# Kernel tuning notes

Measured on AMD Instinct MI355X. Metric: run time of the kernel, lower is better.

## Reference

```python
import jax, jax.numpy as jnp
import numpy as np

B, I, L, D, E, H, HR, A = 4096, 512, 128, 512, 8, 512, 256, 32


def setup_inputs() -> dict:
    key = jax.random.key(0)
    ks = jax.random.split(key, 12)
    s = 0.05
    n = lambda k, shape: (jax.random.normal(k, shape, jnp.float32) * s)
    return {
        "x": jax.random.normal(ks[0], (B, I), jnp.float32),
        "lang_embs": jax.random.normal(ks[1], (B, L), jnp.float32),
        "h_router": jnp.zeros((B, HR), jnp.float32),
        "h_experts": jnp.zeros((E, B, H), jnp.float32),
        # input projection Linear(I+L -> D)
        "W_in": n(ks[2], (D, I + L)), "b_in": jnp.zeros((D,), jnp.float32),
        # router GRU cell (PyTorch layout: rows ordered [r, z, n])
        "Wih_r": n(ks[3], (3 * HR, D)), "Whh_r": n(ks[4], (3 * HR, HR)),
        "bih_r": jnp.zeros((3 * HR,), jnp.float32), "bhh_r": jnp.zeros((3 * HR,), jnp.float32),
        # router fc Linear(HR -> E)
        "W_fc": n(ks[5], (E, HR)), "b_fc": jnp.zeros((E,), jnp.float32),
        # stacked expert GRU cells
        "Wih_e": n(ks[6], (E, 3 * H, D)), "Whh_e": n(ks[7], (E, 3 * H, H)),
        "bih_e": jnp.zeros((E, 3 * H), jnp.float32), "bhh_e": jnp.zeros((E, 3 * H), jnp.float32),
        # stacked expert projections Linear(H -> D)
        "W_proj": n(ks[8], (E, D, H)), "b_proj": jnp.zeros((E, D), jnp.float32),
        # head Linear(D -> A)
        "W_head": n(ks[9], (A, D)), "b_head": jnp.zeros((A,), jnp.float32),
    }


def _gru_cell(gx, gh, h):
    """Single GRU step given precomputed input/hidden gate pre-activations.
    gx, gh: (..., 3H) ordered [r, z, n]; h: (..., H)."""
    Hh = h.shape[-1]
    r = jax.nn.sigmoid(gx[..., :Hh] + gh[..., :Hh])
    z = jax.nn.sigmoid(gx[..., Hh:2 * Hh] + gh[..., Hh:2 * Hh])
    nct = jnp.tanh(gx[..., 2 * Hh:] + r * gh[..., 2 * Hh:])
    return (1.0 - z) * nct + z * h


def reference(x, lang_embs, h_router, h_experts,
              W_in, b_in, Wih_r, Whh_r, bih_r, bhh_r, W_fc, b_fc,
              Wih_e, Whh_e, bih_e, bhh_e, W_proj, b_proj, W_head, b_head):
    # input projection: (B, I+L) -> (B, D)
    xp = jnp.concatenate([x, lang_embs], axis=1) @ W_in.T + b_in

    # router GRU step + softmax weights
    gx_r = xp @ Wih_r.T + bih_r                      # (B, 3HR)
    gh_r = h_router @ Whh_r.T + bhh_r                # (B, 3HR)
    h_router_new = _gru_cell(gx_r, gh_r, h_router)   # (B, HR)
    weights = jax.nn.softmax(h_router_new @ W_fc.T + b_fc, axis=-1)  # (B, E)

    # all expert GRU steps fused into batched einsums over the expert dim
    gx_e = jnp.einsum('bd,egd->ebg', xp, Wih_e) + bih_e[:, None, :]        # (E, B, 3H)
    gh_e = jnp.einsum('ebh,egh->ebg', h_experts, Whh_e) + bhh_e[:, None, :]
    h_experts_new = _gru_cell(gx_e, gh_e, h_experts)                        # (E, B, H)

    # per-expert projection back to intermediate dim, then router-weighted sum
    expert_out = jnp.einsum('ebh,edh->ebd', h_experts_new, W_proj) + b_proj[:, None, :]
    combined = jnp.einsum('ebd,be->bd', expert_out, weights)               # (B, D)

    logits = combined @ W_head.T + b_head                                  # (B, A)
    return (logits, h_router_new, h_experts_new)
```

## Files before the change

### kernel.cpp

```cpp
#include <hip/hip_runtime.h>
#include <cstddef>
#include <cstdint>

#define B_  4096
#define I_  512
#define L_  128
#define D_  512
#define E_  8
#define H_  512
#define HR_ 256
#define A_  32

typedef __attribute__((ext_vector_type(8))) __bf16 bf16x8;
typedef __attribute__((ext_vector_type(4))) __bf16 bf16x4;
typedef __attribute__((ext_vector_type(4))) float floatx4;

__device__ __forceinline__ float sigmoidf_(float x) { return 1.0f / (1.0f + __expf(-x)); }

__device__ __forceinline__ void load_lds16(const void* g, void* l) {
    __builtin_amdgcn_global_load_lds((__attribute__((address_space(1))) void*)g,
                                     (__attribute__((address_space(3))) void*)l, 16, 0, 0);
}

struct HiLo { __bf16 h, l; };
__device__ __forceinline__ HiLo hi_lo(float v) {
    HiLo r;
    r.h = (__bf16)v;
    r.l = (__bf16)(v - (float)r.h);
    return r;
}
__device__ __forceinline__ void split4(float4 v, bf16x4& hi, bf16x4& lo) {
    HiLo a = hi_lo(v.x), b = hi_lo(v.y), c = hi_lo(v.z), d = hi_lo(v.w);
    hi = (bf16x4){a.h, b.h, c.h, d.h};
    lo = (bf16x4){a.l, b.l, c.l, d.l};
}

__global__ __launch_bounds__(256) void f2b_k(const float* __restrict__ src,
                                             __bf16* __restrict__ dst, int n4) {
    int i = blockIdx.x * 256 + threadIdx.x;
    if (i < n4) {
        float4 v = ((const float4*)src)[i];
        bf16x4 o = { (__bf16)v.x, (__bf16)v.y, (__bf16)v.z, (__bf16)v.w };
        *(bf16x4*)(dst + (size_t)i * 4) = o;
    }
}

__global__ __launch_bounds__(256) void wcat2_k(const float* __restrict__ W,
                                               __bf16* __restrict__ out,
                                               int K4, int n4tot) {
    int i4 = blockIdx.x * 256 + threadIdx.x;
    if (i4 >= n4tot) return;
    int row = i4 / K4;
    int c4  = i4 - row * K4;
    const int K = K4 * 4;
    float4 v = ((const float4*)W)[i4];
    bf16x4 hi, lo;
    split4(v, hi, lo);
    __bf16* dst = out + (size_t)row * 2 * K + c4 * 4;
    *(bf16x4*)(dst)     = hi;
    *(bf16x4*)(dst + K) = lo;
}

__global__ __launch_bounds__(256) void concat_cat_k(const float* __restrict__ x,
                                                    const float* __restrict__ lang,
                                                    __bf16* __restrict__ out) {
    int idx = blockIdx.x * 256 + threadIdx.x;
    int b = idx / 160;
    int c = idx - b * 160;
    float4 v;
    if (c < 128) v = ((const float4*)x)[(size_t)b * 128 + c];
    else         v = ((const float4*)lang)[(size_t)b * 32 + (c - 128)];
    bf16x4 hi, lo;
    split4(v, hi, lo);
    __bf16* dst = out + (size_t)b * 1920 + c * 4;
    *(bf16x4*)(dst)        = hi;
    *(bf16x4*)(dst + 640)  = hi;
    *(bf16x4*)(dst + 1280) = lo;
}

__global__ __launch_bounds__(256) void split2cat_k(const float* __restrict__ src,
                                                   __bf16* __restrict__ out) {
    int i4 = blockIdx.x * 256 + threadIdx.x;
    int b = i4 >> 7;
    int c4 = i4 & 127;
    float4 v = ((const float4*)src)[i4];
    bf16x4 hi, lo;
    split4(v, hi, lo);
    __bf16* dst = out + (size_t)b * 1536 + c4 * 4;
    *(bf16x4*)(dst)         = hi;
    *(bf16x4*)(dst + 512)   = hi;
    *(bf16x4*)(dst + 1024)  = lo;
}

__global__ __launch_bounds__(256) void f2bhe_k(const float* __restrict__ he,
                                               __bf16* __restrict__ dst, int r0) {
    int i4 = blockIdx.x * 256 + threadIdx.x;
    int e   = i4 >> 18;
    int rem = i4 & 262143;
    int row = rem >> 7;
    int c4  = rem & 127;
    float4 v = ((const float4*)he)[(size_t)e * (B_ * 128) + (size_t)(r0 + row) * 128 + c4];
    bf16x4 o = { (__bf16)v.x, (__bf16)v.y, (__bf16)v.z, (__bf16)v.w };
    *(bf16x4*)(dst + (size_t)i4 * 4) = o;
}

template<int MODE, bool XORD>
__global__ __launch_bounds__(256) void mgemm(
    const __bf16* __restrict__ A, long long aBatch,
    const __bf16* __restrict__ Bw, long long bBatch, int bRS, int kWrap,
    const float* __restrict__ bias, long long biasBatch,
    float* __restrict__ Cv, long long cBatch,
    int N, int K,
    const float* __restrict__ scale, int sstride, int szBatch)
{
    constexpr int ASZ = 128 * 32;
    __shared__ __align__(16) __bf16 As[2 * ASZ];
    __shared__ __align__(16) __bf16 Bs[2 * ASZ];

    const int tid  = threadIdx.x;
    const int w    = tid >> 6;
    const int lane = tid & 63;
    const int m0 = (XORD ? blockIdx.z : blockIdx.x) * 128;
    const int n0 = blockIdx.y * 128;
    const int z  = XORD ? blockIdx.x : blockIdx.z;

    const int lrow = lane >> 2;
    const int lseg = lane & 3;
    const __bf16* Ag0 = A + (size_t)z * aBatch + (size_t)(m0 + w * 32 + lrow) * K + lseg * 8;
    const __bf16* Ag1 = Ag0 + (size_t)16 * K;
    const __bf16* Bg0 = Bw + (size_t)z * bBatch + (size_t)(n0 + w * 32 + lrow) * bRS + lseg * 8;
    const __bf16* Bg1 = Bg0 + (size_t)16 * bRS;

    const int wm = w & 1, wn = w >> 1;
    const int lr16 = lane & 15;
    const int lq   = lane >> 4;

    floatx4 acc[4][4];
#pragma unroll
    for (int i = 0; i < 4; ++i)
#pragma unroll
        for (int j = 0; j < 4; ++j) acc[i][j] = (floatx4){0.f, 0.f, 0.f, 0.f};

    const int NSTEP = K >> 5;

    auto STAGE = [&](int s, int buf) {
        const int k0 = s << 5;
        const int kb = (k0 < kWrap) ? k0 : (k0 - kWrap);
        __bf16* al = As + buf * ASZ + (w * 32) * 32;
        __bf16* bl = Bs + buf * ASZ + (w * 32) * 32;
        load_lds16(Ag0 + k0, al);
        load_lds16(Ag1 + k0, al + 16 * 32);
        load_lds16(Bg0 + kb, bl);
        load_lds16(Bg1 + kb, bl + 16 * 32);
    };

    int cur = 0;
    STAGE(0, 0);
    __syncthreads();
    for (int s = 0; s < NSTEP; ++s) {
        if (s + 1 < NSTEP) STAGE(s + 1, cur ^ 1);

        const __bf16* Af = As + cur * ASZ + (wm * 64 + lr16) * 32 + lq * 8;
        const __bf16* Bf = Bs + cur * ASZ + (wn * 64 + lr16) * 32 + lq * 8;
        bf16x8 af[4], bfr[4];
#pragma unroll
        for (int t = 0; t < 4; ++t) {
            af[t]  = *(const bf16x8*)(Af + t * 16 * 32);
            bfr[t] = *(const bf16x8*)(Bf + t * 16 * 32);
        }
#pragma unroll
        for (int tm = 0; tm < 4; ++tm)
#pragma unroll
            for (int tn = 0; tn < 4; ++tn)
                acc[tm][tn] = __builtin_amdgcn_mfma_f32_16x16x32_bf16(af[tm], bfr[tn], acc[tm][tn], 0, 0, 0);

        __syncthreads();
        cur ^= 1;
    }

    const float* biasz = bias + (size_t)z * biasBatch;
    const int sz = z * szBatch;
#pragma unroll
    for (int tm = 0; tm < 4; ++tm) {
        const int mbase = m0 + wm * 64 + tm * 16 + lq * 4;
#pragma unroll
        for (int r = 0; r < 4; ++r) {
            const int m = mbase + r;
            float wsc = 0.f;
            if (MODE == 2) wsc = scale[(size_t)m * sstride + sz];
#pragma unroll
            for (int tn = 0; tn < 4; ++tn) {
                const int n = n0 + wn * 64 + tn * 16 + lr16;
                float v = acc[tm][tn][r] + biasz[n];
                const size_t ci = (size_t)z * cBatch + (size_t)m * N + n;
                if (MODE == 0) Cv[ci] = v;
                else           Cv[ci] = wsc * v;
            }
        }
    }
}

template<int HD, bool WRITE_HNEW, bool XORD>
__global__ __launch_bounds__(256) void fgru(
    const __bf16* __restrict__ Ab, long long aBatch,
    const __bf16* __restrict__ Whh, long long wBatch,
    const float* __restrict__ bhh, long long bhhBatch,
    const float* __restrict__ gx, long long gxBatch,
    const float* __restrict__ hprev, long long hBatch,
    float* __restrict__ hout, long long hoBatch,
    __bf16* __restrict__ hnew, long long hnBatch)
{
    __shared__ __align__(16) __bf16 As[128 * 32];
    __shared__ __align__(16) __bf16 Bs[192 * 32];

    const int tid  = threadIdx.x;
    const int w    = tid >> 6;
    const int lane = tid & 63;
    const int m0 = (XORD ? blockIdx.z : blockIdx.x) * 128;
    const int j0 = blockIdx.y * 64;
    const int z  = XORD ? blockIdx.x : blockIdx.z;

    const int lrow = lane >> 2;
    const int lseg = lane & 3;
    const __bf16* Ag0 = Ab + (size_t)z * aBatch + (size_t)(m0 + w * 32 + lrow) * HD + lseg * 8;
    const __bf16* Ag1 = Ag0 + (size_t)16 * HD;
    __bf16* Al0 = As + (w * 32) * 32;
    __bf16* Al1 = Al0 + 16 * 32;

    const __bf16* Wz = Whh + (size_t)z * wBatch;
    const __bf16* Bg[3];
    __bf16* Bl[3];
#pragma unroll
    for (int i = 0; i < 3; ++i) {
        const int r = (w * 3 + i) * 16 + lrow;
        const int gate = r >> 6;
        const int grow = gate * HD + j0 + (r & 63);
        Bg[i] = Wz + (size_t)grow * HD + lseg * 8;
        Bl[i] = Bs + ((w * 3 + i) * 16) * 32;
    }

    const int mh = w & 1, nh = w >> 1;
    const int lr16 = lane & 15;
    const int lq   = lane >> 4;
    const __bf16* Af = As + (mh * 64 + lr16) * 32 + lq * 8;
    const __bf16* Bf = Bs + (nh * 32 + lr16) * 32 + lq * 8;

    floatx4 acc[3][4][2];
#pragma unroll
    for (int g = 0; g < 3; ++g)
#pragma unroll
        for (int i = 0; i < 4; ++i)
#pragma unroll
            for (int j = 0; j < 2; ++j) acc[g][i][j] = (floatx4){0.f, 0.f, 0.f, 0.f};

    for (int k0 = 0; k0 < HD; k0 += 32) {
        __syncthreads();
        load_lds16(Ag0 + k0, Al0);
        load_lds16(Ag1 + k0, Al1);
#pragma unroll
        for (int i = 0; i < 3; ++i) load_lds16(Bg[i] + k0, Bl[i]);
        __syncthreads();

        bf16x8 af[4], bf[3][2];
#pragma unroll
        for (int t = 0; t < 4; ++t) af[t] = *(const bf16x8*)(Af + t * 16 * 32);
#pragma unroll
        for (int g = 0; g < 3; ++g)
#pragma unroll
            for (int tn = 0; tn < 2; ++tn)
                bf[g][tn] = *(const bf16x8*)(Bf + (g * 64 + tn * 16) * 32);
#pragma unroll
        for (int g = 0; g < 3; ++g)
#pragma unroll
            for (int tm = 0; tm < 4; ++tm)
#pragma unroll
                for (int tn = 0; tn < 2; ++tn)
                    acc[g][tm][tn] = __builtin_amdgcn_mfma_f32_16x16x32_bf16(af[tm], bf[g][tn], acc[g][tm][tn], 0, 0, 0);
    }

    const float* bhhz = bhh + (size_t)z * bhhBatch;
#pragma unroll
    for (int tm = 0; tm < 4; ++tm) {
#pragma unroll
        for (int rr = 0; rr < 4; ++rr) {
            const int row = m0 + mh * 64 + tm * 16 + lq * 4 + rr;
            const float* gxrow = gx + (size_t)z * gxBatch + (size_t)row * (3 * HD);
            const float* hrow  = hprev + (size_t)z * hBatch + (size_t)row * HD;
#pragma unroll
            for (int tn = 0; tn < 2; ++tn) {
                const int j = j0 + nh * 32 + tn * 16 + lr16;
                float ghr = acc[0][tm][tn][rr] + bhhz[j];
                float ghz = acc[1][tm][tn][rr] + bhhz[HD + j];
                float ghn = acc[2][tm][tn][rr] + bhhz[2 * HD + j];
                float r  = sigmoidf_(gxrow[j] + ghr);
                float zz = sigmoidf_(gxrow[HD + j] + ghz);
                float n  = tanhf(gxrow[2 * HD + j] + r * ghn);
                float hv = hrow[j];
                float o  = (1.f - zz) * n + zz * hv;
                hout[(size_t)z * hoBatch + (size_t)row * HD + j] = o;
                if (WRITE_HNEW)
                    hnew[(size_t)z * hnBatch + (size_t)row * HD + j] = (__bf16)o;
            }
        }
    }
}

template<int MROWS>
__global__ __launch_bounds__(256, 2) void fxgru_k(
    const __bf16* __restrict__ xpc,
    const __bf16* __restrict__ Wih,
    const float* __restrict__ bih,
    const __bf16* __restrict__ heb,
    const __bf16* __restrict__ Whh,
    const float* __restrict__ bhh,
    const float* __restrict__ hprev,
    long long hBatch,
    float* __restrict__ hout,
    long long hoBatch,
    __bf16* __restrict__ hnew)
{
    constexpr int ASZ = 128 * 32;
    constexpr int BSZ = 192 * 32;
    __shared__ __align__(16) __bf16 As[2 * ASZ];
    __shared__ __align__(16) __bf16 Bs[2 * BSZ];

    const int tid  = threadIdx.x;
    const int w    = tid >> 6;
    const int lane = tid & 63;
    const int z  = blockIdx.x;
    const int j0 = blockIdx.y * 64;
    const int m0 = blockIdx.z * 128;

    const int lrow = lane >> 2;
    const int lseg = lane & 3;
    const int aoff = (w * 32) * 32;
    int BlOff[3];
#pragma unroll
    for (int i = 0; i < 3; ++i) BlOff[i] = ((w * 3 + i) * 16) * 32;

    const int mh = w & 1, nh = w >> 1;
    const int lr16 = lane & 15;
    const int lq   = lane >> 4;

    floatx4 acc[3][4][2];
    floatx4 accn[4][2];
#pragma unroll
    for (int g = 0; g < 3; ++g)
#pragma unroll
        for (int i = 0; i < 4; ++i)
#pragma unroll
            for (int j = 0; j < 2; ++j) acc[g][i][j] = (floatx4){0.f, 0.f, 0.f, 0.f};
#pragma unroll
    for (int i = 0; i < 4; ++i)
#pragma unroll
        for (int j = 0; j < 2; ++j) accn[i][j] = (floatx4){0.f, 0.f, 0.f, 0.f};

    auto COMPA = [&](int buf) {
        const __bf16* Af = As + buf * ASZ + (mh * 64 + lr16) * 32 + lq * 8;
        const __bf16* Bf = Bs + buf * BSZ + (nh * 32 + lr16) * 32 + lq * 8;
        bf16x8 af[4], bf[3][2];
#pragma unroll
        for (int t = 0; t < 4; ++t) af[t] = *(const bf16x8*)(Af + t * 16 * 32);
#pragma unroll
        for (int g = 0; g < 3; ++g)
#pragma unroll
            for (int tn = 0; tn < 2; ++tn)
                bf[g][tn] = *(const bf16x8*)(Bf + (g * 64 + tn * 16) * 32);
#pragma unroll
        for (int g = 0; g < 3; ++g)
#pragma unroll
            for (int tm = 0; tm < 4; ++tm)
#pragma unroll
                for (int tn = 0; tn < 2; ++tn)
                    acc[g][tm][tn] = __builtin_amdgcn_mfma_f32_16x16x32_bf16(af[tm], bf[g][tn], acc[g][tm][tn], 0, 0, 0);
    };
    auto COMPB = [&](int buf) {
        const __bf16* Af = As + buf * ASZ + (mh * 64 + lr16) * 32 + lq * 8;
        const __bf16* Bf = Bs + buf * BSZ + (nh * 32 + lr16) * 32 + lq * 8;
        bf16x8 af[4], bf[3][2];
#pragma unroll
        for (int t = 0; t < 4; ++t) af[t] = *(const bf16x8*)(Af + t * 16 * 32);
#pragma unroll
        for (int g = 0; g < 3; ++g)
#pragma unroll
            for (int tn = 0; tn < 2; ++tn)
                bf[g][tn] = *(const bf16x8*)(Bf + (g * 64 + tn * 16) * 32);
#pragma unroll
        for (int tm = 0; tm < 4; ++tm)
#pragma unroll
            for (int tn = 0; tn < 2; ++tn) {
                acc[0][tm][tn] = __builtin_amdgcn_mfma_f32_16x16x32_bf16(af[tm], bf[0][tn], acc[0][tm][tn], 0, 0, 0);
                acc[1][tm][tn] = __builtin_amdgcn_mfma_f32_16x16x32_bf16(af[tm], bf[1][tn], acc[1][tm][tn], 0, 0, 0);
                accn[tm][tn]   = __builtin_amdgcn_mfma_f32_16x16x32_bf16(af[tm], bf[2][tn], accn[tm][tn], 0, 0, 0);
            }
    };

    int cur = 0;
    {
        const __bf16* AgA0 = xpc + (size_t)(m0 + w * 32 + lrow) * 1536 + lseg * 8;
        const __bf16* AgA1 = AgA0 + (size_t)16 * 1536;
        const __bf16* WihZ = Wih + (size_t)z * (1536 * 1024);
        const __bf16* BgA[3];
#pragma unroll
        for (int i = 0; i < 3; ++i) {
            const int r = (w * 3 + i) * 16 + lrow;
            const int grow = (r >> 6) * 512 + j0 + (r & 63);
            BgA[i] = WihZ + (size_t)grow * 1024 + lseg * 8;
        }
        auto STAGE_A = [&](int s, int buf) {
            const int k0 = s << 5;
            const int kb = (k0 < 1024) ? k0 : (k0 - 1024);
            __bf16* al = As + buf * ASZ + aoff;
            __bf16* bl = Bs + buf * BSZ;
            load_lds16(AgA0 + k0, al);
            load_lds16(AgA1 + k0, al + 16 * 32);
#pragma unroll
            for (int i = 0; i < 3; ++i) load_lds16(BgA[i] + kb, bl + BlOff[i]);
        };

        STAGE_A(0, 0);
        __syncthreads();
        for (int s = 0; s < 47; ++s) {
            STAGE_A(s + 1, cur ^ 1);
            COMPA(cur);
            __syncthreads();
            cur ^= 1;
        }
    }
    {
        const __bf16* AgB0 = heb + (size_t)z * (MROWS * 512)
                                 + (size_t)(m0 + w * 32 + lrow) * 512 + lseg * 8;
        const __bf16* AgB1 = AgB0 + (size_t)16 * 512;
        const __bf16* WhhZ = Whh + (size_t)z * (1536 * 512);
        const __bf16* BgB[3];
#pragma unroll
        for (int i = 0; i < 3; ++i) {
            const int r = (w * 3 + i) * 16 + lrow;
            const int grow = (r >> 6) * 512 + j0 + (r & 63);
            BgB[i] = WhhZ + (size_t)grow * 512 + lseg * 8;
        }
        auto STAGE_B = [&](int t, int buf) {
            const int k0 = t << 5;
            __bf16* al = As + buf * ASZ + aoff;
            __bf16* bl = Bs + buf * BSZ;
            load_lds16(AgB0 + k0, al);
            load_lds16(AgB1 + k0, al + 16 * 32);
#pragma unroll
            for (int i = 0; i < 3; ++i) load_lds16(BgB[i] + k0, bl + BlOff[i]);
        };

        STAGE_B(0, cur ^ 1);
        COMPA(cur);
        __syncthreads();
        cur ^= 1;
        for (int t = 0; t < 16; ++t) {
            if (t + 1 < 16) STAGE_B(t + 1, cur ^ 1);
            COMPB(cur);
            __syncthreads();
            cur ^= 1;
        }
    }

    const float* bihz = bih + (size_t)z * 1536;
    const float* bhhz = bhh + (size_t)z * 1536;
#pragma unroll
    for (int tm = 0; tm < 4; ++tm) {
#pragma unroll
        for (int rr = 0; rr < 4; ++rr) {
            const int row = m0 + mh * 64 + tm * 16 + lq * 4 + rr;
            const float* hrow = hprev + (size_t)z * hBatch + (size_t)row * 512;
#pragma unroll
            for (int tn = 0; tn < 2; ++tn) {
                const int j = j0 + nh * 32 + tn * 16 + lr16;
                float gr  = acc[0][tm][tn][rr] + bihz[j] + bhhz[j];
                float gz  = acc[1][tm][tn][rr] + bihz[512 + j] + bhhz[512 + j];
                float gxn = acc[2][tm][tn][rr] + bihz[1024 + j];
                float ghn = accn[tm][tn][rr] + bhhz[1024 + j];
                float r  = sigmoidf_(gr);
                float zz = sigmoidf_(gz);
                float n  = tanhf(gxn + r * ghn);
                float hv = hrow[j];
                float o  = (1.f - zz) * n + zz * hv;
                hout[(size_t)z * hoBatch + (size_t)row * 512 + j] = o;
                hnew[(size_t)z * (MROWS * 512) + (size_t)row * 512 + j] = (__bf16)o;
            }
        }
    }
}

__global__ __launch_bounds__(256) void fc_softmax_k(const float* __restrict__ hr,
                                                    const float* __restrict__ Wfc,
                                                    const float* __restrict__ bfc,
                                                    float* __restrict__ wts) {
    int lane = threadIdx.x & 63;
    int wave = threadIdx.x >> 6;
    int rg = lane >> 3;
    int e  = lane & 7;
    int b  = blockIdx.x * 32 + wave * 8 + rg;
    const float* h = hr + (size_t)b * HR_;
    const float* w = Wfc + (size_t)e * HR_;
    float acc = 0.0f;
#pragma unroll 4
    for (int k = 0; k < HR_; k += 4) {
        float4 hv = *(const float4*)(h + k);
        float4 wv = *(const float4*)(w + k);
        acc += hv.x * wv.x + hv.y * wv.y + hv.z * wv.z + hv.w * wv.w;
    }
    acc += bfc[e];
    float m = acc;
    for (int off = 4; off; off >>= 1) m = fmaxf(m, __shfl_xor(m, off, 8));
    float ex = __expf(acc - m);
    float s = ex;
    for (int off = 4; off; off >>= 1) s += __shfl_xor(s, off, 8);
    wts[(size_t)b * E_ + e] = ex / s;
}

__global__ __launch_bounds__(256) void reduce8_k(const float* __restrict__ P,
                                                 float* __restrict__ comb,
                                                 int n4, int ps4) {
    int i = blockIdx.x * 256 + threadIdx.x;
    if (i >= n4) return;
    float4 s = ((const float4*)P)[i];
#pragma unroll
    for (int e = 1; e < E_; ++e) {
        float4 v = ((const float4*)P)[i + (size_t)e * ps4];
        s.x += v.x; s.y += v.y; s.z += v.z; s.w += v.w;
    }
    ((float4*)comb)[i] = s;
}

__global__ __launch_bounds__(256) void head_k(const float* __restrict__ comb,
                                              const float* __restrict__ Wh,
                                              const float* __restrict__ bh,
                                              float* __restrict__ out) {
    __shared__ float hs[8][512];
    int b0 = blockIdx.x * 8;
    for (int i = threadIdx.x; i < 8 * 128; i += 256) {
        int rr = i >> 7, cc = i & 127;
        ((float4*)hs[rr])[cc] = ((const float4*)(comb + (size_t)(b0 + rr) * 512))[cc];
    }
    __syncthreads();
    int r = threadIdx.x >> 5, c = threadIdx.x & 31;
    const float* wrow = Wh + (size_t)c * 512;
    float acc = 0.f;
    for (int k = 0; k < 512; k += 4) {
        float4 wv = *(const float4*)(wrow + k);
        float4 hv = *(const float4*)(&hs[r][k]);
        acc += hv.x * wv.x + hv.y * wv.y + hv.z * wv.z + hv.w * wv.w;
    }
    out[(size_t)(b0 + r) * 32 + c] = acc + bh[c];
}

extern "C" void kernel_launch(void* const* d_in, const int* in_sizes, int n_in,
                              void* d_out, int out_size, void* d_ws, size_t ws_size,
                              hipStream_t stream)
{
    const float* x      = (const float*)d_in[0];
    const float* lang   = (const float*)d_in[1];
    const float* h_r    = (const float*)d_in[2];
    const float* h_e    = (const float*)d_in[3];
    const float* W_in   = (const float*)d_in[4];
    const float* b_in   = (const float*)d_in[5];
    const float* Wih_r  = (const float*)d_in[6];
    const float* Whh_r  = (const float*)d_in[7];
    const float* bih_r  = (const float*)d_in[8];
    const float* bhh_r  = (const float*)d_in[9];
    const float* W_fc   = (const float*)d_in[10];
    const float* b_fc   = (const float*)d_in[11];
    const float* Wih_e  = (const float*)d_in[12];
    const float* Whh_e  = (const float*)d_in[13];
    const float* bih_e  = (const float*)d_in[14];
    const float* bhh_e  = (const float*)d_in[15];
    const float* W_proj = (const float*)d_in[16];
    const float* b_proj = (const float*)d_in[17];
    const float* W_head = (const float*)d_in[18];
    const float* b_head = (const float*)d_in[19];

    float* out_logits = (float*)d_out;
    float* out_hr     = out_logits + (size_t)B_ * A_;
    float* out_he     = out_hr + (size_t)B_ * HR_;

    char* wsb = (char*)d_ws;
    size_t off = 0;
    auto alloc = [&](size_t bytes) -> char* {
        char* p = wsb + off;
        off = (off + bytes + 255) & ~(size_t)255;
        return p;
    };

    __bf16* Wih_e_hl = (__bf16*)alloc((size_t)12288 * 1024 * 2);
    __bf16* Whh_e_b  = (__bf16*)alloc((size_t)8 * 1536 * 512 * 2);
    __bf16* W_proj_b = (__bf16*)alloc((size_t)8 * 512 * 512 * 2);
    __bf16* xp_cat   = (__bf16*)alloc((size_t)B_ * 1536 * 2);
    float*  wts      = (float*)alloc((size_t)B_ * E_ * 4);
    float*  comb     = (float*)alloc((size_t)B_ * D_ * 4);

    char* R = wsb + off;
    __bf16* W_in_hl  = (__bf16*)(R);
    __bf16* Wih_r_hl = (__bf16*)(R + 1310720);
    __bf16* Whh_r_b  = (__bf16*)(R + 1310720 + 1572864);
    __bf16* hr_b     = (__bf16*)(R + 1310720 + 1572864 + 393216);
    char*   Rp       = R + 1310720 + 1572864 + 393216 + 2097152;
    __bf16* xcat_cat = (__bf16*)(Rp);
    float*  xp       = (float*)(Rp + 15728640);
    float*  gxr      = (float*)(Rp + 15728640 + 8388608);
    float*  Pch      = (float*)(R);
    __bf16* hebch    = (__bf16*)(R + 33554432);
    __bf16* henewch  = (__bf16*)(R + 33554432 + 16777216);

    wcat2_k<<<(512 * 160 + 255) / 256, 256, 0, stream>>>(W_in, W_in_hl, 160, 512 * 160);
    wcat2_k<<<(768 * 128 + 255) / 256, 256, 0, stream>>>(Wih_r, Wih_r_hl, 128, 768 * 128);
    wcat2_k<<<(12288 * 128 + 255) / 256, 256, 0, stream>>>(Wih_e, Wih_e_hl, 128, 12288 * 128);
    f2b_k<<<(49152 + 255) / 256, 256, 0, stream>>>(Whh_r, Whh_r_b, 49152);
    f2b_k<<<(1572864 + 255) / 256, 256, 0, stream>>>(Whh_e, Whh_e_b, 1572864);
    f2b_k<<<(524288 + 255) / 256, 256, 0, stream>>>(W_proj, W_proj_b, 524288);
    f2b_k<<<(262144 + 255) / 256, 256, 0, stream>>>(h_r, hr_b, 262144);

    concat_cat_k<<<(B_ * 160) / 256, 256, 0, stream>>>(x, lang, xcat_cat);
    mgemm<0, false><<<dim3(32, 4, 1), 256, 0, stream>>>(xcat_cat, 0, W_in_hl, 0, 1280, 1280,
                                                        b_in, 0, xp, 0, D_, 1920, nullptr, 0, 0);
    split2cat_k<<<(B_ * 128) / 256, 256, 0, stream>>>(xp, xp_cat);

    mgemm<0, false><<<dim3(32, 6, 1), 256, 0, stream>>>(xp_cat, 0, Wih_r_hl, 0, 1024, 1024,
                                                        bih_r, 0, gxr, 0, 3 * HR_, 1536, nullptr, 0, 0);
    fgru<HR_, false, false><<<dim3(32, 4, 1), 256, 0, stream>>>(
        hr_b, 0, Whh_r_b, 0, bhh_r, 0, gxr, 0, h_r, 0, out_hr, 0, nullptr, 0);
    fc_softmax_k<<<B_ / 32, 256, 0, stream>>>(out_hr, W_fc, b_fc, wts);

    for (int c = 0; c < 2; ++c) {
        const int r0 = c * 2048;
        f2bhe_k<<<(8 * 2048 * 128) / 256, 256, 0, stream>>>(h_e, hebch, r0);
        fxgru_k<2048><<<dim3(8, 8, 16), 256, 0, stream>>>(
            xp_cat + (size_t)r0 * 1536,
            Wih_e_hl, bih_e,
            hebch, Whh_e_b, bhh_e,
            h_e + (size_t)r0 * H_, (long long)B_ * H_,
            out_he + (size_t)r0 * H_, (long long)B_ * H_,
            henewch);
        mgemm<2, true><<<dim3(8, 4, 16), 256, 0, stream>>>(
            henewch, (long long)2048 * H_,
            W_proj_b, (long long)D_ * H_, 512, 512,
            b_proj, D_,
            Pch, (long long)2048 * D_, D_, H_,
            wts + (size_t)r0 * E_, E_, 1);
        reduce8_k<<<(2048 * 128 + 255) / 256, 256, 0, stream>>>(
            Pch, comb + (size_t)r0 * D_, 2048 * 128, 2048 * 128);
    }

    head_k<<<B_ / 8, 256, 0, stream>>>(comb, W_head, b_head, out_logits);
}
```

Baseline: 719.7 us.

## Triple-buffer LDS tiles in fused expert GRU GEMM with vmcnt-based waits

Expands the shared-memory A/B tile buffers from two to three stages and prefetches two tiles ahead. Full __syncthreads are replaced with explicit vmcnt waits plus raw barriers, so async global-to-LDS loads overlap longer with MFMA compute. The input-gate and hidden-gate phases are chained through the same ring buffer with an explicit drain at the end. This costs more LDS per block, which could limit occupancy, and relies on correct hand-counted vmcnt values.

Measured after the change: 675.8 us. 1.06x faster.

```diff
diff --git a/kernel.cpp b/kernel.cpp
--- a/kernel.cpp
+++ b/kernel.cpp
@@ -321,8 +321,8 @@
 {
     constexpr int ASZ = 128 * 32;
     constexpr int BSZ = 192 * 32;
-    __shared__ __align__(16) __bf16 As[2 * ASZ];
-    __shared__ __align__(16) __bf16 Bs[2 * BSZ];
+    __shared__ __align__(16) __bf16 As[3 * ASZ];
+    __shared__ __align__(16) __bf16 Bs[3 * BSZ];
 
     const int tid  = threadIdx.x;
     const int w    = tid >> 6;
@@ -395,6 +395,16 @@
             }
     };
 
+#define TILE_WAIT(N) do { \
+        asm volatile("s_waitcnt vmcnt(" #N ")" ::: "memory"); \
+        __builtin_amdgcn_s_barrier(); \
+        __builtin_amdgcn_sched_barrier(0); \
+    } while (0)
+#define READ_DONE() do { \
+        __builtin_amdgcn_sched_barrier(0); \
+        __builtin_amdgcn_s_barrier(); \
+    } while (0)
+
     int cur = 0;
     {
         const __bf16* AgA0 = xpc + (size_t)(m0 + w * 32 + lrow) * 1536 + lseg * 8;
@@ -419,12 +429,14 @@
         };
 
         STAGE_A(0, 0);
-        __syncthreads();
-        for (int s = 0; s < 47; ++s) {
-            STAGE_A(s + 1, cur ^ 1);
+        STAGE_A(1, 1);
+        STAGE_A(2, 2);
+        for (int s = 0; s < 45; ++s) {
+            TILE_WAIT(10);
             COMPA(cur);
-            __syncthreads();
-            cur ^= 1;
+            READ_DONE();
+            STAGE_A(s + 3, cur);
+            cur = (cur == 2) ? 0 : cur + 1;
         }
     }
     {
@@ -449,17 +461,32 @@
             for (int i = 0; i < 3; ++i) load_lds16(BgB[i] + k0, bl + BlOff[i]);
         };
 
-        STAGE_B(0, cur ^ 1);
-        COMPA(cur);
-        __syncthreads();
-        cur ^= 1;
-        for (int t = 0; t < 16; ++t) {
-            if (t + 1 < 16) STAGE_B(t + 1, cur ^ 1);
+#pragma unroll
+        for (int q = 0; q < 3; ++q) {
+            TILE_WAIT(10);
+            COMPA(cur);
+            READ_DONE();
+            STAGE_B(q, cur);
+            cur = (cur == 2) ? 0 : cur + 1;
+        }
+        for (int t = 0; t < 13; ++t) {
+            TILE_WAIT(10);
             COMPB(cur);
-            __syncthreads();
-            cur ^= 1;
-        }
-    }
+            READ_DONE();
+            STAGE_B(t + 3, cur);
+            cur = (cur == 2) ? 0 : cur + 1;
+        }
+        TILE_WAIT(10);
+        COMPB(cur);
+        cur = (cur == 2) ? 0 : cur + 1;
+        TILE_WAIT(5);
+        COMPB(cur);
+        cur = (cur == 2) ? 0 : cur + 1;
+        TILE_WAIT(0);
+        COMPB(cur);
+    }
+#undef TILE_WAIT
+#undef READ_DONE
 
     const float* bihz = bih + (size_t)z * 1536;
     const float* bhhz = bhh + (size_t)z * 1536;
```
